# Kernel tuning notes

Measured on AMD Instinct MI355X. Metric: run time of the kernel, lower is better.

Reference implementation:

```python
import jax, jax.numpy as jnp
import numpy as np

B, S, N, D, NAMED, NTYPES = 8, 64, 100, 1024, 768, 5

def _ln(x, g, b, eps=1e-5):
    m = x.mean(-1, keepdims=True)
    v = ((x - m) ** 2).mean(-1, keepdims=True)
    return (x - m) * jax.lax.rsqrt(v + eps) * g + b

def _lin(x, W, b=None):
    y = x @ W.T
    return y if b is None else y + b

def setup_inputs():
    key = jax.random.key(0)
    ks = jax.random.split(key, 24)
    p = lambda i, shape, s=0.02: jax.random.normal(ks[i], shape, jnp.float32) * s
    inp = {}
    inp['scene_reps'] = jax.random.normal(ks[0], (B, S, D), jnp.float32)
    u = jax.random.uniform(ks[1], (B, N, S))
    keep = (jax.random.uniform(ks[2], (B, N, S)) < 0.25).astype(jnp.float32)
    inp['incidence_matrix'] = u * keep
    inp['edge_type_ids'] = jax.random.randint(ks[3], (B, S), 0, NTYPES)
    inp['entity_type_ids'] = jax.random.randint(ks[4], (B, N), 0, NTYPES)
    inp['entity_mask'] = jax.random.uniform(ks[5], (B, N)) < 0.9
    inp['entity_name_embs'] = jax.random.normal(ks[6], (B, N, NAMED), jnp.float32)
    inp['type_embed'] = p(7, (NTYPES, D), 1.0)
    inp['name_W'] = p(8, (D, NAMED))
    inp['name_ln_g'] = jnp.ones(D); inp['name_ln_b'] = jnp.zeros(D)
    inp['n2e_W'] = p(9, (D, D)); inp['n2e_b'] = jnp.zeros(D)
    inp['t2e_W'] = p(10, (D, D)); inp['t2e_b'] = jnp.zeros(D)
    inp['edge_ln_g'] = jnp.ones(D); inp['edge_ln_b'] = jnp.zeros(D)
    inp['gate_W1'] = p(11, (D // 4, D)); inp['gate_b1'] = jnp.zeros(D // 4)
    inp['gate_W2'] = p(12, (3, D // 4)); inp['gate_b2'] = jnp.zeros(3)
    inp['ms_W'] = p(13, (D, D)); inp['ms_b'] = jnp.zeros(D)
    inp['ma_W'] = p(14, (D, D)); inp['ma_b'] = jnp.zeros(D)
    inp['mi_W'] = p(15, (D, D)); inp['mi_b'] = jnp.zeros(D)
    inp['role_w'] = p(16, (D,))
    inp['gru_Wih'] = p(17, (3 * D, D)); inp['gru_Whh'] = p(18, (3 * D, D))
    inp['gru_bih'] = jnp.zeros(3 * D); inp['gru_bhh'] = jnp.zeros(3 * D)
    inp['upd_ln_g'] = jnp.ones(D); inp['upd_ln_b'] = jnp.zeros(D)
    inp['eo_W'] = p(19, (D, D)); inp['eo_b'] = jnp.zeros(D)
    inp['eo_ln_g'] = jnp.ones(D); inp['eo_ln_b'] = jnp.zeros(D)
    inp['res_ln_g'] = jnp.ones(D); inp['res_ln_b'] = jnp.zeros(D)
    return inp

def reference(scene_reps, incidence_matrix, edge_type_ids, entity_type_ids, entity_mask, entity_name_embs, type_embed, name_W, name_ln_g, name_ln_b, n2e_W, n2e_b, t2e_W, t2e_b, edge_ln_g, edge_ln_b, gate_W1, gate_b1, gate_W2, gate_b2, ms_W, ms_b, ma_W, ma_b, mi_W, mi_b, role_w, gru_Wih, gru_Whh, gru_bih, gru_bhh, upd_ln_g, upd_ln_b, eo_W, eo_b, eo_ln_g, eo_ln_b, res_ln_g, res_ln_b):
    # edge_type_ids is accepted by the torch module but unused in its forward.
    dt = scene_reps.dtype
    emaskf = entity_mask.astype(dt)  # [B,N]
    h0 = type_embed[entity_type_ids] + _ln(_lin(entity_name_embs, name_W), name_ln_g, name_ln_b)
    h0 = h0 * emaskf[..., None]
    eye = jnp.eye(N, dtype=dt)
    step_ids = jnp.arange(S)

    def step(carry, xs):
        h, ebuf = carry  # h [B,N,D], ebuf [B,S,D] (hyperedge history)
        s, x_s, inc_s = xs  # x_s [B,D], inc_s [B,N]
        roles = inc_s * emaskf
        wsum = jnp.maximum(roles.sum(1, keepdims=True), 1.0)
        mean_ent = jnp.einsum('bn,bnd->bd', roles, h) / wsum
        e_s = _ln(_lin(mean_ent, n2e_W, n2e_b) + _lin(x_s, t2e_W, t2e_b), edge_ln_g, edge_ln_b)
        in_mask = (roles > 0).astype(dt)[..., None]  # [B,N,1]
        msg_scene = _lin(e_s, ms_W, ms_b)[:, None, :]
        # arc stream: attention over past hyperedges with exponential recency decay
        valid = (step_ids < s).astype(dt)
        denom = jnp.maximum(s - 1, 1).astype(dt)
        decay = jnp.exp(-1.0 + step_ids.astype(dt) / denom) * valid  # linspace(-1,0,s)
        arc = incidence_matrix * roles[:, :, None] * decay[None, None, :]  # [B,N,S]
        arc = arc / jnp.maximum(arc.sum(-1, keepdims=True), 1e-8)
        msg_arc = _lin(jnp.einsum('bns,bsd->bnd', arc, jax.lax.stop_gradient(ebuf)), ma_W, ma_b)
        msg_arc = jnp.where(s > 0, msg_arc, jnp.zeros_like(msg_arc))
        # interaction stream: entity co-occurrence within the scene
        co = roles[:, :, None] * roles[:, None, :] * (1.0 - eye)
        co = co / jnp.maximum(co.sum(-1, keepdims=True), 1e-8)
        msg_int = _lin(jnp.einsum('bnm,bmd->bnd', co, h), mi_W, mi_b)
        gate = jax.nn.softmax(_lin(jax.nn.gelu(_lin(e_s, gate_W1, gate_b1), approximate=False), gate_W2, gate_b2), axis=-1)  # [B,3]
        msg = gate[:, 0, None, None] * msg_scene + gate[:, 1, None, None] * msg_arc + gate[:, 2, None, None] * msg_int
        msg = msg + (roles[..., None] * role_w) * in_mask
        # GRUCell (torch semantics) + LayerNorm, masked update
        gi = _lin(msg, gru_Wih, gru_bih)
        gh = _lin(h, gru_Whh, gru_bhh)
        i_r, i_z, i_n = jnp.split(gi, 3, axis=-1)
        h_r, h_z, h_n = jnp.split(gh, 3, axis=-1)
        r = jax.nn.sigmoid(i_r + h_r)
        z = jax.nn.sigmoid(i_z + h_z)
        n = jnp.tanh(i_n + r * h_n)
        h_new = jnp.clip(_ln((1 - z) * n + z * h, upd_ln_g, upd_ln_b), -50.0, 50.0)
        h = h * (1 - in_mask) + h_new * in_mask
        ebuf = ebuf.at[:, s].set(e_s)
        return (h, ebuf), e_s

    ebuf0 = jnp.zeros((B, S, D), dt)
    (h_fin, _), es = jax.lax.scan(step, (h0, ebuf0), (step_ids, scene_reps.transpose(1, 0, 2), incidence_matrix.transpose(2, 0, 1)))
    H = es.transpose(1, 0, 2)  # [B,S,D]
    H = _ln(H + scene_reps, res_ln_g, res_ln_b)
    H = _ln(jax.nn.gelu(_lin(H, eo_W, eo_b), approximate=False), eo_ln_g, eo_ln_b)
    return (H, h_fin)
```

## Files before the change

### kernel.cpp

```cpp
#include <hip/hip_runtime.h>
#include <math.h>

#define B_   8
#define S_   64
#define N_   100
#define D_   1024
#define ND_  768
#define BN_  800
#define G3_  3072
#define HC7  7168
#define RSC  0.00390625f

typedef _Float16 f16x8 __attribute__((ext_vector_type(8)));
typedef float f32x4 __attribute__((ext_vector_type(4)));

#define MFMA16(a,b,c) __builtin_amdgcn_mfma_f32_16x16x32_f16(a, b, c, 0, 0, 0)

static __device__ __forceinline__ float wave_sum(float v) {
    for (int off = 32; off > 0; off >>= 1) v += __shfl_down(v, off, 64);
    return v;
}

static __device__ __forceinline__ float wave_allsum(float v) {
    for (int off = 1; off < 64; off <<= 1) v += __shfl_xor(v, off, 64);
    return v;
}

static __device__ __forceinline__ float block_sum(float v) {
    __shared__ float red_[8];
    float w = wave_sum(v);
    int lane = threadIdx.x & 63, wid = threadIdx.x >> 6;
    __syncthreads();
    if (lane == 0) red_[wid] = w;
    __syncthreads();
    float t = 0.f;
    for (int i = 0; i < 4; ++i) t += red_[i];
    return t;
}

static __device__ __forceinline__ float gelu_f(float x) {
    return 0.5f * x * (1.f + erff(x * 0.70710678118654752f));
}

static __device__ __forceinline__ unsigned short f2h(float x) {
    union { _Float16 h; unsigned short u; } c; c.h = (_Float16)x; return c.u;
}

__global__ __launch_bounds__(256) void k_f2h(
    const float* __restrict__ src, unsigned short* __restrict__ dst,
    int rows, int cols, int ldd)
{
    size_t n = (size_t)rows * cols;
    size_t i = ((size_t)blockIdx.x * 256 + threadIdx.x) * 4;
    if (i >= n) return;
    int r = (int)(i / cols);
    int c = (int)(i - (size_t)r * cols);
    float4 v = *(const float4*)(src + i);
    ushort4 o; o.x = f2h(v.x); o.y = f2h(v.y); o.z = f2h(v.z); o.w = f2h(v.w);
    *(ushort4*)(dst + (size_t)r * ldd + c) = o;
}

__global__ __launch_bounds__(256) void k_f2hT(
    const float* __restrict__ src, unsigned short* __restrict__ dst,
    int R, int C, int ldd, int rowoff)
{
    __shared__ _Float16 T[32][33];
    int tr = threadIdx.x >> 3, tc4 = (threadIdx.x & 7) * 4;
    int r0 = blockIdx.y * 32, c0 = blockIdx.x * 32;
    float4 v = *(const float4*)(src + (size_t)(r0 + tr) * C + c0 + tc4);
    T[tc4][tr] = (_Float16)v.x; T[tc4+1][tr] = (_Float16)v.y;
    T[tc4+2][tr] = (_Float16)v.z; T[tc4+3][tr] = (_Float16)v.w;
    __syncthreads();
    union { _Float16 h; unsigned short u; } cv;
    ushort4 o;
    cv.h = T[tr][tc4];   o.x = cv.u;
    cv.h = T[tr][tc4+1]; o.y = cv.u;
    cv.h = T[tr][tc4+2]; o.z = cv.u;
    cv.h = T[tr][tc4+3]; o.w = cv.u;
    *(ushort4*)(dst + (size_t)(rowoff + c0 + tr) * ldd + r0 + tc4) = o;
}

__global__ __launch_bounds__(256) void k_mfma16_nt(
    const unsigned short* __restrict__ A16, const unsigned short* __restrict__ W16,
    const float* __restrict__ bias, float* __restrict__ C,
    unsigned short* __restrict__ C16, float oscale,
    int M, int Nc, int K)
{
    int m0 = blockIdx.y * 64; if (m0 >= M) return;
    int n0 = blockIdx.x * 128;
    __shared__ _Float16 sA[64][72];
    __shared__ _Float16 sB[128][72];
    int tid = threadIdx.x;
    int w = tid >> 6, l = tid & 63;
    int l15 = l & 15, q = l >> 4;
    int wn = w * 32;
    int arow = tid >> 3, achk = (tid & 7) * 8;
    f32x4 acc[4][2] = {};
    for (int k0 = 0; k0 < K; k0 += 64) {
        for (int ri = 0; ri < 64; ri += 32) {
            int gm = m0 + arow + ri;
            uint4 v = make_uint4(0u, 0u, 0u, 0u);
            if (gm < M) v = *(const uint4*)(A16 + (size_t)gm * K + k0 + achk);
            *(uint4*)(&sA[arow + ri][achk]) = v;
        }
        for (int i = 0; i < 4; ++i) {
            int r = arow + 32 * i;
            *(uint4*)(&sB[r][achk]) = *(const uint4*)(W16 + (size_t)(n0 + r) * K + k0 + achk);
        }
        __syncthreads();
#pragma unroll
        for (int ks = 0; ks < 64; ks += 32) {
            f16x8 b0 = *(const f16x8*)(&sB[wn + l15][ks + q*8]);
            f16x8 b1 = *(const f16x8*)(&sB[wn + 16 + l15][ks + q*8]);
#pragma unroll
            for (int mi = 0; mi < 4; ++mi) {
                f16x8 a = *(const f16x8*)(&sA[mi*16 + l15][ks + q*8]);
                acc[mi][0] = MFMA16(a, b0, acc[mi][0]);
                acc[mi][1] = MFMA16(a, b1, acc[mi][1]);
            }
        }
        __syncthreads();
    }
    for (int mi = 0; mi < 4; ++mi)
        for (int nj = 0; nj < 2; ++nj)
            for (int r = 0; r < 4; ++r) {
                int gm = m0 + mi*16 + q*4 + r;
                int cl = wn + nj*16 + l15;
                if (gm < M) {
                    size_t off = (size_t)gm * Nc + n0 + cl;
                    float v = acc[mi][nj][r];
                    if (C16) C16[off] = f2h(v * oscale);
                    else C[off] = v + (bias ? bias[n0 + cl] : 0.f);
                }
            }
}

__global__ __launch_bounds__(256) void k_h0(
    const float* __restrict__ P, const int* __restrict__ etype,
    const int* __restrict__ emask, const float* __restrict__ temb,
    const float* __restrict__ g, const float* __restrict__ bt,
    float* __restrict__ h, unsigned short* __restrict__ h16)
{
    int bn = blockIdx.x, tid = threadIdx.x;
    int t = etype[bn], mk = emask[bn];
    float x[4]; float lsum = 0.f;
    for (int k = 0; k < 4; ++k) { x[k] = P[(size_t)bn*D_ + tid + 256*k]; lsum += x[k]; }
    float mean = block_sum(lsum) * (1.f / D_);
    float lv = 0.f;
    for (int k = 0; k < 4; ++k) { float d = x[k] - mean; lv += d * d; }
    float inv = rsqrtf(block_sum(lv) * (1.f / D_) + 1e-5f);
    for (int k = 0; k < 4; ++k) {
        int d = tid + 256*k;
        float y = (x[k] - mean) * inv * g[d] + bt[d];
        float hv = mk ? (temb[(size_t)t*D_ + d] + y) : 0.f;
        h[(size_t)bn*D_ + d] = hv;
        h16[(size_t)bn*D_ + d] = f2h(hv);
    }
}

__global__ __launch_bounds__(256) void k_hcat0(
    const unsigned short* __restrict__ h16, const unsigned short* __restrict__ n2e16,
    const unsigned short* __restrict__ Wmi16, const unsigned short* __restrict__ Whh16,
    float* __restrict__ Hcat)
{
    int m0 = blockIdx.y * 32;
    int n0 = blockIdx.x * 64;
    const unsigned short* Bp; int ldb; int nl;
    if (n0 < 1024)      { Bp = n2e16;        ldb = D_;  nl = n0; }
    else if (n0 < 4096) { Bp = Wmi16 + 2048; ldb = G3_; nl = n0 - 1024; }
    else                { Bp = Whh16;        ldb = D_;  nl = n0 - 4096; }
    __shared__ _Float16 sA[32][72];
    __shared__ _Float16 sB[64][72];
    int tid = threadIdx.x;
    int w = tid >> 6, l = tid & 63;
    int l15 = l & 15, q = l >> 4;
    int wm = (w & 1) * 16, wn = (w >> 1) * 32;
    int arow = tid >> 3, achk = (tid & 7) * 8;
    int gmA = m0 + arow;
    f32x4 acc[2] = {};
    for (int k0 = 0; k0 < D_; k0 += 64) {
        *(uint4*)(&sA[arow][achk]) = *(const uint4*)(h16 + (size_t)gmA*D_ + k0 + achk);
        *(uint4*)(&sB[arow][achk])      = *(const uint4*)(Bp + (size_t)(nl + arow)*ldb + k0 + achk);
        *(uint4*)(&sB[arow + 32][achk]) = *(const uint4*)(Bp + (size_t)(nl + arow + 32)*ldb + k0 + achk);
        __syncthreads();
#pragma unroll
        for (int ks = 0; ks < 64; ks += 32) {
            f16x8 a  = *(const f16x8*)(&sA[wm + l15][ks + q*8]);
            f16x8 b0 = *(const f16x8*)(&sB[wn + l15][ks + q*8]);
            f16x8 b1 = *(const f16x8*)(&sB[wn + 16 + l15][ks + q*8]);
            acc[0] = MFMA16(a, b0, acc[0]);
            acc[1] = MFMA16(a, b1, acc[1]);
        }
        __syncthreads();
    }
    for (int j = 0; j < 2; ++j)
        for (int r = 0; r < 4; ++r) {
            int row = wm + q*4 + r;
            Hcat[(size_t)(m0 + row)*HC7 + n0 + wn + j*16 + l15] = acc[j][r];
        }
}

__global__ __launch_bounds__(256) void k_front(
    const float* __restrict__ inc, const int* __restrict__ emask,
    const float* __restrict__ Esmi, float* __restrict__ arcsum,
    int* __restrict__ cntp, int* __restrict__ lst, float* __restrict__ rro,
    float* __restrict__ scl,
    const int* __restrict__ prevcnt, const int* __restrict__ prevlist,
    const unsigned short* __restrict__ h16, const unsigned short* __restrict__ n2e16,
    const unsigned short* __restrict__ Wmi16, const unsigned short* __restrict__ Whh16,
    float* __restrict__ Hcat, float* __restrict__ gatepre,
    float* __restrict__ esumP, float* __restrict__ TmiP, float* __restrict__ wsumP,
    int s)
{
    int tid = threadIdx.x, bid = blockIdx.x;
    if (bid == 0 && tid < 32) gatepre[tid] = 0.f;
    if (bid < BN_) {
        int m = bid;
        int b = m / N_;
        float r = emask[m] ? inc[(size_t)m*S_ + s] : 0.f;
        if (r <= 0.f) return;
        __shared__ int sidx, nwa;
        __shared__ float wav[S_]; __shared__ int wai[S_];
        if (tid == 0) { sidx = atomicAdd(cntp, 1); nwa = 0; }
        __syncthreads();
        int idx = sidx;
        float denomA = fmaxf((float)(s - 1), 1.f);
        float wa = 0.f;
        if (tid < s) {
            float iv = inc[(size_t)m*S_ + tid];
            if (iv > 0.f) {
                wa = iv * r * expf(-1.f + (float)tid / denomA);
                int p = atomicAdd(&nwa, 1);
                wav[p] = wa; wai[p] = tid;
            }
        }
        float dA = block_sum(wa);
        float rm = 0.f;
        if (tid < N_) rm = emask[b*N_ + tid] ? inc[((size_t)b*N_ + tid)*S_ + s] : 0.f;
        float wsum = block_sum(rm);
        __syncthreads();
        int na = nwa;
        float sclA = 1.f / fmaxf(dA, 1e-8f);
        if (tid == 0) {
            lst[idx] = m; rro[idx] = r;
            scl[idx] = r / fmaxf(r * (wsum - r), 1e-8f);
            wsumP[b] = wsum;
        }
        float rprev = (s > 0) ? inc[(size_t)m*S_ + (s-1)] : 0.f;
        if (rprev <= 0.f) {
            const float4* hp = (const float4*)(Hcat + (size_t)m*HC7);
#pragma unroll
            for (int j2 = 0; j2 < 4; ++j2) {
                float4 hv = hp[tid + 256*j2];
                int c = (tid + 256*j2) * 4;
                float* dst = (c < 1024) ? (esumP + (size_t)b*D_ + c)
                                        : (TmiP + (size_t)b*G3_ + (c - 1024));
                atomicAdd(dst + 0, r*hv.x); atomicAdd(dst + 1, r*hv.y);
                atomicAdd(dst + 2, r*hv.z); atomicAdd(dst + 3, r*hv.w);
            }
        }
        f32x4 a4[3];
#pragma unroll
        for (int k = 0; k < 3; ++k) a4[k] = (f32x4){0.f,0.f,0.f,0.f};
        for (int j = 0; j < na; ++j) {
            float wj = wav[j];
            const f32x4* ep = (const f32x4*)(Esmi + ((size_t)b*S_ + wai[j])*G3_);
#pragma unroll
            for (int k = 0; k < 3; ++k) {
                f32x4 e = ep[tid + 256*k];
#pragma unroll
                for (int q = 0; q < 4; ++q) a4[k][q] += wj * e[q];
            }
        }
        f32x4* ao = (f32x4*)(arcsum + (size_t)idx*G3_);
#pragma unroll
        for (int k = 0; k < 3; ++k) {
            f32x4 v;
#pragma unroll
            for (int q = 0; q < 4; ++q) v[q] = a4[k][q] * sclA;
            ao[tid + 256*k] = v;
        }
    } else {
        int pM = *prevcnt;
        int t = bid - BN_;
        int nt = t % 112, mt = t / 112;
        int m0 = mt * 32;
        if (m0 >= pM) return;
        int n0 = nt * 64;
        const unsigned short* Bp; int ldb; int nl;
        if (n0 < 1024)      { Bp = n2e16;        ldb = D_;  nl = n0; }
        else if (n0 < 4096) { Bp = Wmi16 + 2048; ldb = G3_; nl = n0 - 1024; }
        else                { Bp = Whh16;        ldb = D_;  nl = n0 - 4096; }
        __shared__ _Float16 sA[32][72];
        __shared__ _Float16 sB[64][72];
        __shared__ int slist[32];
        __shared__ float srn[32];
        __shared__ int sbb[32];
        if (tid < 32) {
            int gm = m0 + tid;
            int m = (gm < pM) ? prevlist[gm] : 0;
            slist[tid] = m;
            float rn = 0.f;
            if (gm < pM) rn = emask[m] ? inc[(size_t)m*S_ + s] : 0.f;
            srn[tid] = rn;
            sbb[tid] = m / N_;
        }
        __syncthreads();
        int w = tid >> 6, l = tid & 63;
        int l15 = l & 15, q = l >> 4;
        int wm = (w & 1) * 16, wn = (w >> 1) * 32;
        int arow = tid >> 3, achk = (tid & 7) * 8;
        f32x4 acc[2] = {};
        for (int k0 = 0; k0 < D_; k0 += 64) {
            {
                int gm = m0 + arow;
                uint4 v = make_uint4(0u,0u,0u,0u);
                if (gm < pM) v = *(const uint4*)(h16 + (size_t)slist[arow]*D_ + k0 + achk);
                *(uint4*)(&sA[arow][achk]) = v;
            }
            *(uint4*)(&sB[arow][achk])      = *(const uint4*)(Bp + (size_t)(nl + arow)*ldb + k0 + achk);
            *(uint4*)(&sB[arow + 32][achk]) = *(const uint4*)(Bp + (size_t)(nl + arow + 32)*ldb + k0 + achk);
            __syncthreads();
#pragma unroll
            for (int ks = 0; ks < 64; ks += 32) {
                f16x8 a  = *(const f16x8*)(&sA[wm + l15][ks + q*8]);
                f16x8 b0 = *(const f16x8*)(&sB[wn + l15][ks + q*8]);
                f16x8 b1 = *(const f16x8*)(&sB[wn + 16 + l15][ks + q*8]);
                acc[0] = MFMA16(a, b0, acc[0]);
                acc[1] = MFMA16(a, b1, acc[1]);
            }
            __syncthreads();
        }
        for (int nj = 0; nj < 2; ++nj)
            for (int r4 = 0; r4 < 4; ++r4) {
                int row = wm + q*4 + r4;
                int gm = m0 + row;
                if (gm < pM) {
                    float v = acc[nj][r4];
                    int c = n0 + wn + nj*16 + l15;
                    Hcat[(size_t)slist[row]*HC7 + c] = v;
                    float rn = srn[row];
                    if (rn > 0.f && c < 4096) {
                        float* dst = (c < 1024)
                            ? (esumP + (size_t)sbb[row]*D_ + c)
                            : (TmiP + (size_t)sbb[row]*G3_ + (c - 1024));
                        atomicAdd(dst, rn * v);
                    }
                }
            }
    }
}

__global__ __launch_bounds__(256) void k_mid(
    const float* __restrict__ esumP, const float* __restrict__ wsumP,
    float* __restrict__ esumZ, float* __restrict__ TmiZ, float* __restrict__ wsumZ,
    const float* __restrict__ n2eb, const float* __restrict__ pre_t2e,
    const float* __restrict__ elng, const float* __restrict__ elnb,
    const float* __restrict__ gW1, const float* __restrict__ gb1,
    const float* __restrict__ gW2, const unsigned short* __restrict__ Wmi16,
    float* __restrict__ esbuf, float* __restrict__ gatepre,
    float* __restrict__ Emi, float* __restrict__ Esmi,
    int* __restrict__ ctrl, int par, int s)
{
    int bid = blockIdx.x, tid = threadIdx.x;
    if (bid < 32) {
        __shared__ float se[D_];
        int b = bid >> 2, seg = bid & 3;
        if (bid == 0 && tid == 0) ctrl[1 - par] = 0;
        esumZ[(size_t)b*D_ + seg*256 + tid] = 0.f;
#pragma unroll
        for (int j = 0; j < 3; ++j) TmiZ[(size_t)b*G3_ + seg*768 + j*256 + tid] = 0.f;
        if (seg == 0 && tid == 0) wsumZ[b] = 0.f;
        float invw = 1.f / fmaxf(wsumP[b], 1.f);
        float4 ev = ((const float4*)(esumP + (size_t)b*D_))[tid];
        float4 nb = ((const float4*)n2eb)[tid];
        float4 pt = ((const float4*)(pre_t2e + ((size_t)b*S_ + s)*D_))[tid];
        float x[4] = { ev.x*invw + nb.x + pt.x, ev.y*invw + nb.y + pt.y,
                       ev.z*invw + nb.z + pt.z, ev.w*invw + nb.w + pt.w };
        float mean = block_sum(x[0]+x[1]+x[2]+x[3]) * (1.f / D_);
        float lv = 0.f;
#pragma unroll
        for (int k = 0; k < 4; ++k) { float d = x[k] - mean; lv += d * d; }
        float inv = rsqrtf(block_sum(lv) * (1.f / D_) + 1e-5f);
        float4 lg = ((const float4*)elng)[tid];
        float4 lb = ((const float4*)elnb)[tid];
        float y0 = (x[0]-mean)*inv*lg.x + lb.x;
        float y1 = (x[1]-mean)*inv*lg.y + lb.y;
        float y2 = (x[2]-mean)*inv*lg.z + lb.z;
        float y3 = (x[3]-mean)*inv*lg.w + lb.w;
        int d4 = tid * 4;
        se[d4] = y0; se[d4+1] = y1; se[d4+2] = y2; se[d4+3] = y3;
        if (seg == 0)
            ((float4*)(esbuf + ((size_t)b*S_ + s)*D_))[tid] = make_float4(y0,y1,y2,y3);
        __syncthreads();
        if (tid < 64) {
            int u = seg * 64 + tid;
            float acc = gb1[u];
            const float* w1 = gW1 + (size_t)u * D_;
            for (int j = 0; j < D_; j += 4) {
                float4 w = *(const float4*)(w1 + j);
                acc += w.x*se[j] + w.y*se[j+1] + w.z*se[j+2] + w.w*se[j+3];
            }
            float hg = gelu_f(acc);
            for (int c = 0; c < 3; ++c) {
                float p = wave_sum(gW2[c*256 + u] * hg);
                if (tid == 0) atomicAdd(gatepre + b*4 + c, p);
            }
        }
    } else {
        __shared__ float se32[8][1028];
        int w = tid >> 6, lane = tid & 63;
        for (int bb = 0; bb < 2; ++bb) {
            int b = w*2 + bb;
            float invw = 1.f / fmaxf(wsumP[b], 1.f);
            int d0 = lane * 16;
            const float4* ep = (const float4*)(esumP + (size_t)b*D_ + d0);
            const float4* np = (const float4*)(n2eb + d0);
            const float4* pp = (const float4*)(pre_t2e + ((size_t)b*S_ + s)*D_ + d0);
            float x[16]; float sm = 0.f;
#pragma unroll
            for (int j = 0; j < 4; ++j) {
                float4 e = ep[j], n = np[j], p = pp[j];
                x[j*4+0] = e.x*invw + n.x + p.x;
                x[j*4+1] = e.y*invw + n.y + p.y;
                x[j*4+2] = e.z*invw + n.z + p.z;
// ... 16 lines not shown
                se32[b][d0 + j*4 + 3] = (x[j*4+3]-mean)*inv*lg.w + lb.w;
            }
        }
        __syncthreads();
        int t = bid - 32;
        int seg = t & 1;
        int c0 = (t >> 1) * 32;
        int colg = tid >> 5, t31 = tid & 31;
        int cb = c0 + colg * 4;
        float accA[4][8] = {};
#pragma unroll
        for (int i = 0; i < 8; ++i) {
            int kh = t31*4 + i*128;
            float wf[4][4];
#pragma unroll
            for (int c = 0; c < 4; ++c) {
                union { uint2 u; _Float16 h[4]; } cv;
                cv.u = *(const uint2*)(Wmi16 + (size_t)(cb + c)*G3_ + seg*1024 + kh);
                wf[c][0] = (float)cv.h[0]; wf[c][1] = (float)cv.h[1];
                wf[c][2] = (float)cv.h[2]; wf[c][3] = (float)cv.h[3];
            }
#pragma unroll
            for (int b = 0; b < 8; ++b) {
                float4 sv = *(const float4*)(&se32[b][kh]);
#pragma unroll
                for (int c = 0; c < 4; ++c)
                    accA[c][b] += wf[c][0]*sv.x + wf[c][1]*sv.y
                                + wf[c][2]*sv.z + wf[c][3]*sv.w;
            }
        }
#pragma unroll
        for (int off = 16; off >= 1; off >>= 1) {
#pragma unroll
            for (int c = 0; c < 4; ++c)
#pragma unroll
                for (int b = 0; b < 8; ++b)
                    accA[c][b] += __shfl_down(accA[c][b], off, 32);
        }
        if (t31 == 0) {
#pragma unroll
            for (int c = 0; c < 4; ++c) {
                int col = cb + c;
#pragma unroll
                for (int b = 0; b < 8; ++b) {
                    if (seg == 0) Emi[(size_t)b*G3_ + col] = accA[c][b];
                    else Esmi[((size_t)b*S_ + s)*G3_ + col] = accA[c][b];
                }
            }
        }
    }
}

__global__ __launch_bounds__(256) void k_fin(
    const int* __restrict__ lst, const int* __restrict__ cntp,
    const float* __restrict__ rro, const float* __restrict__ scl,
    const float* __restrict__ gatepre, const float* __restrict__ gb2,
    const float* __restrict__ Hcat, const float* __restrict__ Emi,
    const float* __restrict__ arcsum, const float* __restrict__ Tmi,
    const float* __restrict__ gBm, const float* __restrict__ bih,
    const float* __restrict__ bhh,
    const float* __restrict__ ulng, const float* __restrict__ ulnb,
    float* __restrict__ h, unsigned short* __restrict__ h16, int s)
{
    int row = blockIdx.x;
    if (row >= *cntp) return;
    int bn = lst[row];
    int b = bn / N_;
    int tid = threadIdx.x;
    float t0 = gatepre[b*4+0] + gb2[0];
    float t1 = gatepre[b*4+1] + gb2[1];
    float t2 = gatepre[b*4+2] + gb2[2];
    float mx = fmaxf(t0, fmaxf(t1, t2));
    float e0 = expf(t0-mx), e1 = expf(t1-mx), e2 = expf(t2-mx);
    float si = 1.f / (e0 + e1 + e2);
    float g0 = e0*si, g1 = (s > 0) ? e1*si : 0.f, g2 = e2*si;
    float rv = rro[row];
    float sI = scl[row];
    const f32x4* Hmi4 = (const f32x4*)(Hcat + (size_t)bn*HC7 + 1024);
    const f32x4* Hhh4 = (const f32x4*)(Hcat + (size_t)bn*HC7 + 4096);
    const f32x4* em4  = (const f32x4*)(Emi + (size_t)b*G3_);
    const f32x4* as4  = (const f32x4*)(arcsum + (size_t)row*G3_);
    const f32x4* tm4  = (const f32x4*)(Tmi + (size_t)b*G3_);
    const f32x4* gB4  = (const f32x4*)gBm;
    const f32x4* bih4 = (const f32x4*)bih;
    const f32x4* bhh4 = (const f32x4*)bhh;
    const f32x4* h4   = (const f32x4*)(h + (size_t)bn*D_);
    f32x4 ip[3];
#pragma unroll
    for (int c = 0; c < 3; ++c) {
        int dd4 = c*256 + tid;
        f32x4 tm_ = tm4[dd4], hm_ = Hmi4[dd4], em_ = em4[dd4], as_ = as4[dd4];
        f32x4 b0 = gB4[dd4], b1 = gB4[768 + dd4];
        f32x4 b2 = gB4[1536 + dd4], b3 = gB4[2304 + dd4];
        f32x4 bi = bih4[dd4];
#pragma unroll
        for (int j = 0; j < 4; ++j) {
            float gint = tm_[j] - rv * hm_[j];
            ip[c][j] = RSC * (g0*em_[j] + g1*as_[j] + g2*sI*gint)
                     + g0*b0[j] + g1*b1[j] + g2*b2[j] + rv*b3[j] + bi[j];
        }
    }
    f32x4 a0 = Hhh4[tid],       c0 = bhh4[tid];
    f32x4 a1 = Hhh4[256 + tid], c1 = bhh4[256 + tid];
    f32x4 a2 = Hhh4[512 + tid], c2 = bhh4[512 + tid];
    f32x4 hvv = h4[tid];
    f32x4 u4; float lsum = 0.f;
#pragma unroll
    for (int j = 0; j < 4; ++j) {
        float r = 1.f / (1.f + expf(-(ip[0][j] + a0[j] + c0[j])));
        float z = 1.f / (1.f + expf(-(ip[1][j] + a1[j] + c1[j])));
        float nn = tanhf(ip[2][j] + r * (a2[j] + c2[j]));
        u4[j] = (1.f - z) * nn + z * hvv[j];
        lsum += u4[j];
    }
    float mean = block_sum(lsum) * (1.f / D_);
    float lv = 0.f;
#pragma unroll
    for (int j = 0; j < 4; ++j) { float d = u4[j] - mean; lv += d * d; }
    float inv = rsqrtf(block_sum(lv) * (1.f / D_) + 1e-5f);
    f32x4 lg = ((const f32x4*)ulng)[tid];
    f32x4 lb = ((const f32x4*)ulnb)[tid];
    f32x4 y4; ushort4 o;
#pragma unroll
    for (int j = 0; j < 4; ++j) {
        float y = (u4[j] - mean) * inv * lg[j] + lb[j];
        y4[j] = fminf(fmaxf(y, -50.f), 50.f);
    }
    *(f32x4*)(h + (size_t)bn*D_ + tid*4) = y4;
    o.x = f2h(y4[0]); o.y = f2h(y4[1]); o.z = f2h(y4[2]); o.w = f2h(y4[3]);
    *(ushort4*)(h16 + (size_t)bn*D_ + tid*4) = o;
}

__global__ __launch_bounds__(256) void k_resln(
    float* __restrict__ buf, const float* __restrict__ scene,
    const float* __restrict__ g, const float* __restrict__ bt,
    unsigned short* __restrict__ H16)
{
    size_t row = blockIdx.x;
    int tid = threadIdx.x;
    float x[4]; float lsum = 0.f;
    for (int k = 0; k < 4; ++k) {
        int d = tid + 256*k;
        x[k] = buf[row*D_ + d] + scene[row*D_ + d];
        lsum += x[k];
    }
    float mean = block_sum(lsum) * (1.f / D_);
    float lv = 0.f;
    for (int k = 0; k < 4; ++k) { float d = x[k] - mean; lv += d * d; }
    float inv = rsqrtf(block_sum(lv) * (1.f / D_) + 1e-5f);
    for (int k = 0; k < 4; ++k) {
        int d = tid + 256*k;
        float y = (x[k] - mean) * inv * g[d] + bt[d];
        buf[row*D_ + d] = y;
        H16[row*D_ + d] = f2h(y);
    }
}

__global__ __launch_bounds__(256) void k_final(
    const float* __restrict__ G, const float* __restrict__ g, const float* __restrict__ bt,
    float* __restrict__ outH, const float* __restrict__ h, float* __restrict__ outh)
{
    int tid = threadIdx.x;
    if (blockIdx.x < B_*S_) {
        size_t row = blockIdx.x;
        float x[4]; float lsum = 0.f;
        for (int k = 0; k < 4; ++k) {
            x[k] = gelu_f(G[row*D_ + tid + 256*k]);
            lsum += x[k];
        }
        float mean = block_sum(lsum) * (1.f / D_);
        float lv = 0.f;
        for (int k = 0; k < 4; ++k) { float d = x[k] - mean; lv += d * d; }
        float inv = rsqrtf(block_sum(lv) * (1.f / D_) + 1e-5f);
        for (int k = 0; k < 4; ++k) {
            int d = tid + 256*k;
            outH[row*D_ + d] = (x[k] - mean) * inv * g[d] + bt[d];
        }
    } else {
        size_t bn = blockIdx.x - B_*S_;
        for (int d = tid; d < D_; d += 256)
            outh[bn*D_ + d] = h[bn*D_ + d];
    }
}

extern "C" void kernel_launch(void* const* d_in, const int* in_sizes, int n_in,
                              void* d_out, int out_size, void* d_ws, size_t ws_size,
                              hipStream_t stream)
{
    const float* scene = (const float*)d_in[0];
    const float* inc   = (const float*)d_in[1];
    const int*   etype = (const int*)d_in[3];
    const int*   emask = (const int*)d_in[4];
    const float* nemb  = (const float*)d_in[5];
    const float* temb  = (const float*)d_in[6];
    const float* nameW = (const float*)d_in[7];
    const float* nlg   = (const float*)d_in[8];
    const float* nlb   = (const float*)d_in[9];
    const float* n2eW  = (const float*)d_in[10];
    const float* n2eb  = (const float*)d_in[11];
    const float* t2eW  = (const float*)d_in[12];
    const float* t2eb  = (const float*)d_in[13];
    const float* elng  = (const float*)d_in[14];
    const float* elnb  = (const float*)d_in[15];
    const float* gW1   = (const float*)d_in[16];
    const float* gb1   = (const float*)d_in[17];
    const float* gW2   = (const float*)d_in[18];
    const float* gb2   = (const float*)d_in[19];
    const float* msW   = (const float*)d_in[20];
    const float* msB   = (const float*)d_in[21];
    const float* maW   = (const float*)d_in[22];
    const float* maB   = (const float*)d_in[23];
    const float* miW   = (const float*)d_in[24];
    const float* miB   = (const float*)d_in[25];
    const float* rolew = (const float*)d_in[26];
    const float* Wih   = (const float*)d_in[27];
    const float* Whh   = (const float*)d_in[28];
    const float* bih   = (const float*)d_in[29];
    const float* bhh   = (const float*)d_in[30];
    const float* ulng  = (const float*)d_in[31];
    const float* ulnb  = (const float*)d_in[32];
    const float* eoW   = (const float*)d_in[33];
    const float* eoB   = (const float*)d_in[34];
    const float* eolng = (const float*)d_in[35];
    const float* eolnb = (const float*)d_in[36];
    const float* rlng  = (const float*)d_in[37];
    const float* rlnb  = (const float*)d_in[38];

    float* outH = (float*)d_out;
    float* outh = outH + (size_t)B_*S_*D_;

    float* W = (float*)d_ws;
    size_t o = 0;
    int*   ctrl     = (int*)(W + o); o += 64;
    float* esum2    = W + o; o += 2*(size_t)B_*D_;
    float* Tmi2     = W + o; o += 2*(size_t)B_*G3_;
    float* wsum2    = W + o; o += 16;
    float* gatepre  = W + o; o += 32;
    float* rowrole  = W + o; o += 2*BN_;
    float* sclbuf   = W + o; o += BN_;
    int*   list     = (int*)(W + o); o += 2*BN_;
    float* hbuf     = W + o; o += (size_t)BN_*D_;
    float* Hcat     = W + o; o += (size_t)BN_*HC7;
    float* pre_t2e  = W + o; o += (size_t)B_*S_*D_;
    float* gBm      = W + o; o += 4*G3_;
    float* Emi      = W + o; o += (size_t)B_*G3_;
    float* Esmi     = W + o; o += (size_t)B_*S_*G3_;
    float* arcsum   = W + o; o += (size_t)BN_*G3_;
    float* tmp      = W + o; o += (size_t)BN_*D_;
    unsigned short* U = (unsigned short*)(W + o);
    size_t uo = 0;
    unsigned short* h16    = U + uo; uo += (size_t)BN_*D_;
    unsigned short* H16    = U + uo; uo += (size_t)B_*S_*D_;
    unsigned short* Wih16  = U + uo; uo += (size_t)G3_*D_;
    unsigned short* Whh16  = U + uo; uo += (size_t)G3_*D_;
    unsigned short* n2e16  = U + uo; uo += (size_t)D_*D_;
    unsigned short* eoW16  = U + uo; uo += (size_t)D_*D_;
    unsigned short* nW16   = U + uo; uo += (size_t)D_*ND_;
    unsigned short* nE16   = U + uo; uo += (size_t)BN_*ND_;
    unsigned short* t2e16  = U + uo; uo += (size_t)D_*D_;
    unsigned short* sc16   = U + uo; uo += (size_t)B_*S_*D_;
    unsigned short* WcatT16= U + uo; uo += (size_t)G3_*D_;
    unsigned short* Wmi16  = U + uo; uo += (size_t)G3_*G3_;
    unsigned short* bias4  = U + uo; uo += 4*D_;

    hipMemsetAsync(ctrl, 0,
        (64 + 2*(size_t)B_*D_ + 2*(size_t)B_*G3_ + 16) * sizeof(float), stream);

    #define CVT(src, dst, r, c, ld) \
        k_f2h<<<(((size_t)(r)*(c)/4 + 255)/256), 256, 0, stream>>>(src, dst, r, c, ld)
    CVT(Wih,   Wih16, G3_, D_,  D_);
    CVT(Whh,   Whh16, G3_, D_,  D_);
    CVT(n2eW,  n2e16, D_,  D_,  D_);
    CVT(nameW, nW16,  D_,  ND_, ND_);
    CVT(nemb,  nE16,  BN_, ND_, ND_);
    CVT(eoW,   eoW16, D_,  D_,  D_);
    CVT(t2eW,  t2e16, D_,  D_,  D_);
    CVT(scene, sc16,  B_*S_, D_, D_);
    CVT(msB,   bias4 + 0,    1, D_, D_);
    CVT(maB,   bias4 + D_,   1, D_, D_);
    CVT(miB,   bias4 + 2*D_, 1, D_, D_);
    CVT(rolew, bias4 + 3*D_, 1, D_, D_);
    #undef CVT
    k_f2hT<<<dim3(32,32), 256, 0, stream>>>(msW, WcatT16, D_, D_, D_, 0);
    k_f2hT<<<dim3(32,32), 256, 0, stream>>>(maW, WcatT16, D_, D_, D_, D_);
    k_f2hT<<<dim3(32,32), 256, 0, stream>>>(miW, WcatT16, D_, D_, D_, 2*D_);

    k_mfma16_nt<<<dim3(G3_/128, G3_/64), 256, 0, stream>>>(
        Wih16, WcatT16, nullptr, nullptr, Wmi16, 256.f, G3_, G3_, D_);
    k_mfma16_nt<<<dim3(G3_/128, 1), 256, 0, stream>>>(
        bias4, Wih16, nullptr, gBm, nullptr, 1.f, 4, G3_, D_);
    k_mfma16_nt<<<dim3(D_/128, (B_*S_+63)/64), 256, 0, stream>>>(
        sc16, t2e16, t2eb, pre_t2e, nullptr, 1.f, B_*S_, D_, D_);
    k_mfma16_nt<<<dim3(D_/128, (BN_+63)/64), 256, 0, stream>>>(
        nE16, nW16, nullptr, tmp, nullptr, 1.f, BN_, D_, ND_);
    k_h0<<<BN_, 256, 0, stream>>>(tmp, etype, emask, temb, nlg, nlb, hbuf, h16);
    k_hcat0<<<dim3(112, 25), 256, 0, stream>>>(h16, n2e16, Wmi16, Whh16, Hcat);

    for (int s = 0; s < S_; ++s) {
        int par = s & 1;
        int*   cntp = ctrl + par;
        int*   pcnt = ctrl + (1 - par);
        int*   lst  = list + par * BN_;
        int*   plst = list + (1 - par) * BN_;
        float* rro  = rowrole + par * BN_;
        float* esumP = esum2 + (size_t)par * B_*D_;
        float* esumZ = esum2 + (size_t)(1 - par) * B_*D_;
        float* TmiP  = Tmi2 + (size_t)par * B_*G3_;
        float* TmiZ  = Tmi2 + (size_t)(1 - par) * B_*G3_;
        float* wsumP = wsum2 + par * 8;
        float* wsumZ = wsum2 + (1 - par) * 8;
        k_front<<<BN_ + 112*26, 256, 0, stream>>>(inc, emask, Esmi, arcsum,
            cntp, lst, rro, sclbuf, pcnt, plst, h16, n2e16, Wmi16, Whh16,
            Hcat, gatepre, esumP, TmiP, wsumP, s);
        k_mid<<<224, 256, 0, stream>>>(esumP, wsumP, esumZ, TmiZ, wsumZ,
            n2eb, pre_t2e, elng, elnb, gW1, gb1, gW2, Wmi16,
            outH, gatepre, Emi, Esmi, ctrl, par, s);
        k_fin<<<BN_, 256, 0, stream>>>(lst, cntp, rro, sclbuf, gatepre, gb2,
            Hcat, Emi, arcsum, TmiP, gBm, bih, bhh, ulng, ulnb, hbuf, h16, s);
    }

    k_resln<<<B_*S_, 256, 0, stream>>>(outH, scene, rlng, rlnb, H16);
    k_mfma16_nt<<<dim3(D_/128, (B_*S_+63)/64), 256, 0, stream>>>(
        H16, eoW16, eoB, tmp, nullptr, 1.f, B_*S_, D_, D_);
    k_final<<<B_*S_ + BN_, 256, 0, stream>>>(tmp, eolng, eolnb, outH, hbuf, outh);
}
```

Before: 4.033 ms.

## Accumulate role-weighted hidden sums and project once instead of per-row atomics

Instead of projecting every entity's hidden state through n2e and the Wmi slice and then atomically summing the role-weighted outputs into esum/Tmi, the code now accumulates a role-weighted sum of hidden states per batch (hsum) and multiplies that single vector by the weights in extra blocks of k_front. This removes the n2e columns from the per-row Hcat GEMM and removes the large volume of float atomics on 4096-wide outputs. Accumulation moves into k_fin, which now runs for every entity and adds next-step role-weighted fp16 hidden values. The order of rounding changes slightly, and the small GEMV blocks now run alongside the GEMM tiles.

After: 4.988 ms. 23.7% more time.

```diff
diff --git a/kernel.cpp b/kernel.cpp
--- a/kernel.cpp
+++ b/kernel.cpp
@@ -8,7 +8,8 @@
 #define ND_  768
 #define BN_  800
 #define G3_  3072
-#define HC7  7168
+#define HC6  6144
+#define GMB  2400
 #define RSC  0.00390625f
 
 typedef _Float16 f16x8 __attribute__((ext_vector_type(8)));
@@ -44,6 +45,10 @@
 
 static __device__ __forceinline__ unsigned short f2h(float x) {
     union { _Float16 h; unsigned short u; } c; c.h = (_Float16)x; return c.u;
+}
+
+static __device__ __forceinline__ float h2f(unsigned short u) {
+    union { unsigned short u; _Float16 h; } c; c.u = u; return (float)c.h;
 }
 
 __global__ __launch_bounds__(256) void k_f2h(
@@ -139,10 +144,14 @@
     const float* __restrict__ P, const int* __restrict__ etype,
     const int* __restrict__ emask, const float* __restrict__ temb,
     const float* __restrict__ g, const float* __restrict__ bt,
-    float* __restrict__ h, unsigned short* __restrict__ h16)
+    const float* __restrict__ inc,
+    float* __restrict__ h, unsigned short* __restrict__ h16,
+    float* __restrict__ hsum0)
 {
     int bn = blockIdx.x, tid = threadIdx.x;
     int t = etype[bn], mk = emask[bn];
+    int b = bn / N_;
+    float r0 = mk ? inc[(size_t)bn*S_] : 0.f;
     float x[4]; float lsum = 0.f;
     for (int k = 0; k < 4; ++k) { x[k] = P[(size_t)bn*D_ + tid + 256*k]; lsum += x[k]; }
     float mean = block_sum(lsum) * (1.f / D_);
@@ -154,21 +163,22 @@
         float y = (x[k] - mean) * inv * g[d] + bt[d];
         float hv = mk ? (temb[(size_t)t*D_ + d] + y) : 0.f;
         h[(size_t)bn*D_ + d] = hv;
-        h16[(size_t)bn*D_ + d] = f2h(hv);
+        unsigned short us = f2h(hv);
+        h16[(size_t)bn*D_ + d] = us;
+        if (r0 > 0.f) atomicAdd(hsum0 + (size_t)b*D_ + d, r0 * h2f(us));
     }
 }
 
 __global__ __launch_bounds__(256) void k_hcat0(
-    const unsigned short* __restrict__ h16, const unsigned short* __restrict__ n2e16,
+    const unsigned short* __restrict__ h16,
     const unsigned short* __restrict__ Wmi16, const unsigned short* __restrict__ Whh16,
     float* __restrict__ Hcat)
 {
     int m0 = blockIdx.y * 32;
     int n0 = blockIdx.x * 64;
     const unsigned short* Bp; int ldb; int nl;
-    if (n0 < 1024)      { Bp = n2e16;        ldb = D_;  nl = n0; }
-    else if (n0 < 4096) { Bp = Wmi16 + 2048; ldb = G3_; nl = n0 - 1024; }
-    else                { Bp = Whh16;        ldb = D_;  nl = n0 - 4096; }
+    if (n0 < 3072) { Bp = Wmi16 + 2048; ldb = G3_; nl = n0; }
+    else           { Bp = Whh16;        ldb = D_;  nl = n0 - 3072; }
     __shared__ _Float16 sA[32][72];
     __shared__ _Float16 sB[64][72];
     int tid = threadIdx.x;
@@ -196,20 +206,21 @@
     for (int j = 0; j < 2; ++j)
         for (int r = 0; r < 4; ++r) {
             int row = wm + q*4 + r;
-            Hcat[(size_t)(m0 + row)*HC7 + n0 + wn + j*16 + l15] = acc[j][r];
+            Hcat[(size_t)(m0 + row)*HC6 + n0 + wn + j*16 + l15] = acc[j][r];
         }
 }
 
 __global__ __launch_bounds__(256) void k_front(
     const float* __restrict__ inc, const int* __restrict__ emask,
     const float* __restrict__ Esmi, float* __restrict__ arcsum,
-    int* __restrict__ cntp, int* __restrict__ lst, float* __restrict__ rro,
-    float* __restrict__ scl,
+    int* __restrict__ cntp, int* __restrict__ lst, int* __restrict__ invb,
     const int* __restrict__ prevcnt, const int* __restrict__ prevlist,
     const unsigned short* __restrict__ h16, const unsigned short* __restrict__ n2e16,
     const unsigned short* __restrict__ Wmi16, const unsigned short* __restrict__ Whh16,
     float* __restrict__ Hcat, float* __restrict__ gatepre,
-    float* __restrict__ esumP, float* __restrict__ TmiP, float* __restrict__ wsumP,
+    const float* __restrict__ hsumP,
+    float* __restrict__ esum, float* __restrict__ Tmi,
+    float* __restrict__ wsumP,
     int s)
 {
     int tid = threadIdx.x, bid = blockIdx.x;
@@ -242,22 +253,8 @@
         int na = nwa;
         float sclA = 1.f / fmaxf(dA, 1e-8f);
         if (tid == 0) {
-            lst[idx] = m; rro[idx] = r;
-            scl[idx] = r / fmaxf(r * (wsum - r), 1e-8f);
+            lst[idx] = m; invb[m] = idx;
             wsumP[b] = wsum;
-        }
-        float rprev = (s > 0) ? inc[(size_t)m*S_ + (s-1)] : 0.f;
-        if (rprev <= 0.f) {
-            const float4* hp = (const float4*)(Hcat + (size_t)m*HC7);
-#pragma unroll
-            for (int j2 = 0; j2 < 4; ++j2) {
-                float4 hv = hp[tid + 256*j2];
-                int c = (tid + 256*j2) * 4;
-                float* dst = (c < 1024) ? (esumP + (size_t)b*D_ + c)
-                                        : (TmiP + (size_t)b*G3_ + (c - 1024));
-                atomicAdd(dst + 0, r*hv.x); atomicAdd(dst + 1, r*hv.y);
-                atomicAdd(dst + 2, r*hv.z); atomicAdd(dst + 3, r*hv.w);
-            }
         }
         f32x4 a4[3];
 #pragma unroll
@@ -280,30 +277,22 @@
             for (int q = 0; q < 4; ++q) v[q] = a4[k][q] * sclA;
             ao[tid + 256*k] = v;
         }
-    } else {
+    } else if (bid < BN_ + GMB) {
         int pM = *prevcnt;
         int t = bid - BN_;
-        int nt = t % 112, mt = t / 112;
+        int nt = t % 96, mt = t / 96;
         int m0 = mt * 32;
         if (m0 >= pM) return;
         int n0 = nt * 64;
         const unsigned short* Bp; int ldb; int nl;
-        if (n0 < 1024)      { Bp = n2e16;        ldb = D_;  nl = n0; }
-        else if (n0 < 4096) { Bp = Wmi16 + 2048; ldb = G3_; nl = n0 - 1024; }
-        else                { Bp = Whh16;        ldb = D_;  nl = n0 - 4096; }
+        if (n0 < 3072) { Bp = Wmi16 + 2048; ldb = G3_; nl = n0; }
+        else           { Bp = Whh16;        ldb = D_;  nl = n0 - 3072; }
         __shared__ _Float16 sA[32][72];
         __shared__ _Float16 sB[64][72];
         __shared__ int slist[32];
-        __shared__ float srn[32];
-        __shared__ int sbb[32];
         if (tid < 32) {
             int gm = m0 + tid;
-            int m = (gm < pM) ? prevlist[gm] : 0;
-            slist[tid] = m;
-            float rn = 0.f;
-            if (gm < pM) rn = emask[m] ? inc[(size_t)m*S_ + s] : 0.f;
-            srn[tid] = rn;
-            sbb[tid] = m / N_;
+            slist[tid] = (gm < pM) ? prevlist[gm] : 0;
         }
         __syncthreads();
         int w = tid >> 6, l = tid & 63;
@@ -335,25 +324,62 @@
             for (int r4 = 0; r4 < 4; ++r4) {
                 int row = wm + q*4 + r4;
                 int gm = m0 + row;
-                if (gm < pM) {
-                    float v = acc[nj][r4];
-                    int c = n0 + wn + nj*16 + l15;
-                    Hcat[(size_t)slist[row]*HC7 + c] = v;
-                    float rn = srn[row];
-                    if (rn > 0.f && c < 4096) {
-                        float* dst = (c < 1024)
-                            ? (esumP + (size_t)sbb[row]*D_ + c)
-                            : (TmiP + (size_t)sbb[row]*G3_ + (c - 1024));
-                        atomicAdd(dst, rn * v);
-                    }
+                if (gm < pM)
+                    Hcat[(size_t)slist[row]*HC6 + n0 + wn + nj*16 + l15] = acc[nj][r4];
+            }
+    } else {
+        int t2 = bid - (BN_ + GMB);
+        bool epre = (t2 < 32);
+        int c0 = (epre ? t2 : t2 - 32) * 32;
+        int colg = tid >> 5, t31 = tid & 31;
+        int cb = c0 + colg * 4;
+        float acc[4][8] = {};
+#pragma unroll
+        for (int i = 0; i < 8; ++i) {
+            int kh = t31*4 + i*128;
+            float wf[4][4];
+#pragma unroll
+            for (int c = 0; c < 4; ++c) {
+                union { uint2 u; _Float16 hh[4]; } cv;
+                cv.u = epre
+                    ? *(const uint2*)(n2e16 + (size_t)(cb + c)*D_ + kh)
+                    : *(const uint2*)(Wmi16 + (size_t)(cb + c)*G3_ + 2048 + kh);
+                wf[c][0] = (float)cv.hh[0]; wf[c][1] = (float)cv.hh[1];
+                wf[c][2] = (float)cv.hh[2]; wf[c][3] = (float)cv.hh[3];
+            }
+#pragma unroll
+            for (int b = 0; b < 8; ++b) {
+                float4 hv = *(const float4*)(hsumP + (size_t)b*D_ + kh);
+#pragma unroll
+                for (int c = 0; c < 4; ++c)
+                    acc[c][b] += wf[c][0]*hv.x + wf[c][1]*hv.y
+                               + wf[c][2]*hv.z + wf[c][3]*hv.w;
+            }
+        }
+#pragma unroll
+        for (int off = 16; off >= 1; off >>= 1)
+#pragma unroll
+            for (int c = 0; c < 4; ++c)
+#pragma unroll
+                for (int b = 0; b < 8; ++b)
+                    acc[c][b] += __shfl_down(acc[c][b], off, 32);
+        if (t31 == 0) {
+#pragma unroll
+            for (int c = 0; c < 4; ++c) {
+                int col = cb + c;
+#pragma unroll
+                for (int b = 0; b < 8; ++b) {
+                    if (epre) esum[(size_t)b*D_ + col] = acc[c][b];
+                    else Tmi[(size_t)b*G3_ + col] = acc[c][b];
                 }
             }
+        }
     }
 }
 
 __global__ __launch_bounds__(256) void k_mid(
     const float* __restrict__ esumP, const float* __restrict__ wsumP,
-    float* __restrict__ esumZ, float* __restrict__ TmiZ, float* __restrict__ wsumZ,
+    float* __restrict__ hsumZ,
     const float* __restrict__ n2eb, const float* __restrict__ pre_t2e,
     const float* __restrict__ elng, const float* __restrict__ elnb,
     const float* __restrict__ gW1, const float* __restrict__ gb1,
@@ -367,10 +393,7 @@
         __shared__ float se[D_];
         int b = bid >> 2, seg = bid & 3;
         if (bid == 0 && tid == 0) ctrl[1 - par] = 0;
-        esumZ[(size_t)b*D_ + seg*256 + tid] = 0.f;
-#pragma unroll
-        for (int j = 0; j < 3; ++j) TmiZ[(size_t)b*G3_ + seg*768 + j*256 + tid] = 0.f;
-        if (seg == 0 && tid == 0) wsumZ[b] = 0.f;
+        hsumZ[(size_t)b*D_ + seg*256 + tid] = 0.f;
         float invw = 1.f / fmaxf(wsumP[b], 1.f);
         float4 ev = ((const float4*)(esumP + (size_t)b*D_))[tid];
         float4 nb = ((const float4*)n2eb)[tid];
@@ -493,83 +516,103 @@
 }
 
 __global__ __launch_bounds__(256) void k_fin(
-    const int* __restrict__ lst, const int* __restrict__ cntp,
-    const float* __restrict__ rro, const float* __restrict__ scl,
+    const float* __restrict__ inc, const int* __restrict__ emask,
+    const int* __restrict__ invb,
     const float* __restrict__ gatepre, const float* __restrict__ gb2,
     const float* __restrict__ Hcat, const float* __restrict__ Emi,
     const float* __restrict__ arcsum, const float* __restrict__ Tmi,
+    const float* __restrict__ wsumP,
     const float* __restrict__ gBm, const float* __restrict__ bih,
     const float* __restrict__ bhh,
     const float* __restrict__ ulng, const float* __restrict__ ulnb,
-    float* __restrict__ h, unsigned short* __restrict__ h16, int s)
-{
-    int row = blockIdx.x;
-    if (row >= *cntp) return;
-    int bn = lst[row];
-    int b = bn / N_;
+    float* __restrict__ h, unsigned short* __restrict__ h16,
+    float* __restrict__ hsumN, int s)
+{
+    int m = blockIdx.x;
+    int b = m / N_;
     int tid = threadIdx.x;
-    float t0 = gatepre[b*4+0] + gb2[0];
-    float t1 = gatepre[b*4+1] + gb2[1];
-    float t2 = gatepre[b*4+2] + gb2[2];
-    float mx = fmaxf(t0, fmaxf(t1, t2));
-    float e0 = expf(t0-mx), e1 = expf(t1-mx), e2 = expf(t2-mx);
-    float si = 1.f / (e0 + e1 + e2);
-    float g0 = e0*si, g1 = (s > 0) ? e1*si : 0.f, g2 = e2*si;
-    float rv = rro[row];
-    float sI = scl[row];
-    const f32x4* Hmi4 = (const f32x4*)(Hcat + (size_t)bn*HC7 + 1024);
-    const f32x4* Hhh4 = (const f32x4*)(Hcat + (size_t)bn*HC7 + 4096);
-    const f32x4* em4  = (const f32x4*)(Emi + (size_t)b*G3_);
-    const f32x4* as4  = (const f32x4*)(arcsum + (size_t)row*G3_);
-    const f32x4* tm4  = (const f32x4*)(Tmi + (size_t)b*G3_);
-    const f32x4* gB4  = (const f32x4*)gBm;
-    const f32x4* bih4 = (const f32x4*)bih;
-    const f32x4* bhh4 = (const f32x4*)bhh;
-    const f32x4* h4   = (const f32x4*)(h + (size_t)bn*D_);
-    f32x4 ip[3];
-#pragma unroll
-    for (int c = 0; c < 3; ++c) {
-        int dd4 = c*256 + tid;
-        f32x4 tm_ = tm4[dd4], hm_ = Hmi4[dd4], em_ = em4[dd4], as_ = as4[dd4];
-        f32x4 b0 = gB4[dd4], b1 = gB4[768 + dd4];
-        f32x4 b2 = gB4[1536 + dd4], b3 = gB4[2304 + dd4];
-        f32x4 bi = bih4[dd4];
+    float rv = emask[m] ? inc[(size_t)m*S_ + s] : 0.f;
+    float rn = 0.f;
+    if (s + 1 < S_) rn = emask[m] ? inc[(size_t)m*S_ + s + 1] : 0.f;
+    if (rv > 0.f) {
+        int row = invb[m];
+        float wsum = wsumP[b];
+        float sI = rv / fmaxf(rv * (wsum - rv), 1e-8f);
+        float t0 = gatepre[b*4+0] + gb2[0];
+        float t1 = gatepre[b*4+1] + gb2[1];
+        float t2 = gatepre[b*4+2] + gb2[2];
+        float mx = fmaxf(t0, fmaxf(t1, t2));
+        float e0 = expf(t0-mx), e1 = expf(t1-mx), e2 = expf(t2-mx);
+        float si = 1.f / (e0 + e1 + e2);
+        float g0 = e0*si, g1 = (s > 0) ? e1*si : 0.f, g2 = e2*si;
+        const f32x4* Hmi4 = (const f32x4*)(Hcat + (size_t)m*HC6);
+        const f32x4* Hhh4 = (const f32x4*)(Hcat + (size_t)m*HC6 + 3072);
+        const f32x4* em4  = (const f32x4*)(Emi + (size_t)b*G3_);
+        const f32x4* as4  = (const f32x4*)(arcsum + (size_t)row*G3_);
+        const f32x4* tm4  = (const f32x4*)(Tmi + (size_t)b*G3_);
+        const f32x4* gB4  = (const f32x4*)gBm;
+        const f32x4* bih4 = (const f32x4*)bih;
+        const f32x4* bhh4 = (const f32x4*)bhh;
+        const f32x4* h4   = (const f32x4*)(h + (size_t)m*D_);
+        f32x4 ip[3];
+#pragma unroll
+        for (int c = 0; c < 3; ++c) {
+            int dd4 = c*256 + tid;
+            f32x4 tm_ = tm4[dd4], hm_ = Hmi4[dd4], em_ = em4[dd4], as_ = as4[dd4];
+            f32x4 b0 = gB4[dd4], b1 = gB4[768 + dd4];
+            f32x4 b2 = gB4[1536 + dd4], b3 = gB4[2304 + dd4];
+            f32x4 bi = bih4[dd4];
+#pragma unroll
+            for (int j = 0; j < 4; ++j) {
+                float gint = tm_[j] - rv * hm_[j];
+                ip[c][j] = RSC * (g0*em_[j] + g1*as_[j] + g2*sI*gint)
+                         + g0*b0[j] + g1*b1[j] + g2*b2[j] + rv*b3[j] + bi[j];
+            }
+        }
+        f32x4 a0 = Hhh4[tid],       c0 = bhh4[tid];
+        f32x4 a1 = Hhh4[256 + tid], c1 = bhh4[256 + tid];
+        f32x4 a2 = Hhh4[512 + tid], c2 = bhh4[512 + tid];
+        f32x4 hvv = h4[tid];
+        f32x4 u4; float lsum = 0.f;
 #pragma unroll
         for (int j = 0; j < 4; ++j) {
-            float gint = tm_[j] - rv * hm_[j];
-            ip[c][j] = RSC * (g0*em_[j] + g1*as_[j] + g2*sI*gint)
-                     + g0*b0[j] + g1*b1[j] + g2*b2[j] + rv*b3[j] + bi[j];
-        }
-    }
-    f32x4 a0 = Hhh4[tid],       c0 = bhh4[tid];
-    f32x4 a1 = Hhh4[256 + tid], c1 = bhh4[256 + tid];
-    f32x4 a2 = Hhh4[512 + tid], c2 = bhh4[512 + tid];
-    f32x4 hvv = h4[tid];
-    f32x4 u4; float lsum = 0.f;
-#pragma unroll
-    for (int j = 0; j < 4; ++j) {
-        float r = 1.f / (1.f + expf(-(ip[0][j] + a0[j] + c0[j])));
-        float z = 1.f / (1.f + expf(-(ip[1][j] + a1[j] + c1[j])));
-        float nn = tanhf(ip[2][j] + r * (a2[j] + c2[j]));
-        u4[j] = (1.f - z) * nn + z * hvv[j];
-        lsum += u4[j];
-    }
-    float mean = block_sum(lsum) * (1.f / D_);
-    float lv = 0.f;
-#pragma unroll
-    for (int j = 0; j < 4; ++j) { float d = u4[j] - mean; lv += d * d; }
-    float inv = rsqrtf(block_sum(lv) * (1.f / D_) + 1e-5f);
-    f32x4 lg = ((const f32x4*)ulng)[tid];
-    f32x4 lb = ((const f32x4*)ulnb)[tid];
-    f32x4 y4; ushort4 o;
-#pragma unroll
-    for (int j = 0; j < 4; ++j) {
-        float y = (u4[j] - mean) * inv * lg[j] + lb[j];
-        y4[j] = fminf(fmaxf(y, -50.f), 50.f);
-    }
-    *(f32x4*)(h + (size_t)bn*D_ + tid*4) = y4;
-    o.x = f2h(y4[0]); o.y = f2h(y4[1]); o.z = f2h(y4[2]); o.w = f2h(y4[3]);
-    *(ushort4*)(h16 + (size_t)bn*D_ + tid*4) = o;
+            float r = 1.f / (1.f + expf(-(ip[0][j] + a0[j] + c0[j])));
+            float z = 1.f / (1.f + expf(-(ip[1][j] + a1[j] + c1[j])));
+            float nn = tanhf(ip[2][j] + r * (a2[j] + c2[j]));
+            u4[j] = (1.f - z) * nn + z * hvv[j];
+            lsum += u4[j];
+        }
+        float mean = block_sum(lsum) * (1.f / D_);
+        float lv = 0.f;
+#pragma unroll
+        for (int j = 0; j < 4; ++j) { float d = u4[j] - mean; lv += d * d; }
+        float inv = rsqrtf(block_sum(lv) * (1.f / D_) + 1e-5f);
+        f32x4 lg = ((const f32x4*)ulng)[tid];
+        f32x4 lb = ((const f32x4*)ulnb)[tid];
+        f32x4 y4; ushort4 o;
+#pragma unroll
+        for (int j = 0; j < 4; ++j) {
+            float y = (u4[j] - mean) * inv * lg[j] + lb[j];
+            y4[j] = fminf(fmaxf(y, -50.f), 50.f);
+        }
+        *(f32x4*)(h + (size_t)m*D_ + tid*4) = y4;
+        o.x = f2h(y4[0]); o.y = f2h(y4[1]); o.z = f2h(y4[2]); o.w = f2h(y4[3]);
+        *(ushort4*)(h16 + (size_t)m*D_ + tid*4) = o;
+        if (rn > 0.f) {
+            float* dst = hsumN + (size_t)b*D_ + tid*4;
+            atomicAdd(dst + 0, rn * h2f(o.x));
+            atomicAdd(dst + 1, rn * h2f(o.y));
+            atomicAdd(dst + 2, rn * h2f(o.z));
+            atomicAdd(dst + 3, rn * h2f(o.w));
+        }
+    } else if (rn > 0.f) {
+        ushort4 o = *(const ushort4*)(h16 + (size_t)m*D_ + tid*4);
+        float* dst = hsumN + (size_t)b*D_ + tid*4;
+        atomicAdd(dst + 0, rn * h2f(o.x));
+        atomicAdd(dst + 1, rn * h2f(o.y));
+        atomicAdd(dst + 2, rn * h2f(o.z));
+        atomicAdd(dst + 3, rn * h2f(o.w));
+    }
 }
 
 __global__ __launch_bounds__(256) void k_resln(
@@ -673,20 +716,20 @@
     float* W = (float*)d_ws;
     size_t o = 0;
     int*   ctrl     = (int*)(W + o); o += 64;
-    float* esum2    = W + o; o += 2*(size_t)B_*D_;
-    float* Tmi2     = W + o; o += 2*(size_t)B_*G3_;
-    float* wsum2    = W + o; o += 16;
+    float* hsum2    = W + o; o += 2*(size_t)B_*D_;
+    float* wsumB    = W + o; o += 16;
     float* gatepre  = W + o; o += 32;
-    float* rowrole  = W + o; o += 2*BN_;
-    float* sclbuf   = W + o; o += BN_;
     int*   list     = (int*)(W + o); o += 2*BN_;
+    int*   invb     = (int*)(W + o); o += BN_;
     float* hbuf     = W + o; o += (size_t)BN_*D_;
-    float* Hcat     = W + o; o += (size_t)BN_*HC7;
+    float* Hcat     = W + o; o += (size_t)BN_*HC6;
     float* pre_t2e  = W + o; o += (size_t)B_*S_*D_;
     float* gBm      = W + o; o += 4*G3_;
     float* Emi      = W + o; o += (size_t)B_*G3_;
     float* Esmi     = W + o; o += (size_t)B_*S_*G3_;
     float* arcsum   = W + o; o += (size_t)BN_*G3_;
+    float* esum     = W + o; o += (size_t)B_*D_;
+    float* Tmi      = W + o; o += (size_t)B_*G3_;
     float* tmp      = W + o; o += (size_t)BN_*D_;
     unsigned short* U = (unsigned short*)(W + o);
     size_t uo = 0;
@@ -704,8 +747,7 @@
     unsigned short* Wmi16  = U + uo; uo += (size_t)G3_*G3_;
     unsigned short* bias4  = U + uo; uo += 4*D_;
 
-    hipMemsetAsync(ctrl, 0,
-        (64 + 2*(size_t)B_*D_ + 2*(size_t)B_*G3_ + 16) * sizeof(float), stream);
+    hipMemsetAsync(ctrl, 0, (64 + 2*(size_t)B_*D_ + 16) * sizeof(float), stream);
 
     #define CVT(src, dst, r, c, ld) \
         k_f2h<<<(((size_t)(r)*(c)/4 + 255)/256), 256, 0, stream>>>(src, dst, r, c, ld)
@@ -734,30 +776,27 @@
         sc16, t2e16, t2eb, pre_t2e, nullptr, 1.f, B_*S_, D_, D_);
     k_mfma16_nt<<<dim3(D_/128, (BN_+63)/64), 256, 0, stream>>>(
         nE16, nW16, nullptr, tmp, nullptr, 1.f, BN_, D_, ND_);
-    k_h0<<<BN_, 256, 0, stream>>>(tmp, etype, emask, temb, nlg, nlb, hbuf, h16);
-    k_hcat0<<<dim3(112, 25), 256, 0, stream>>>(h16, n2e16, Wmi16, Whh16, Hcat);
+    k_h0<<<BN_, 256, 0, stream>>>(tmp, etype, emask, temb, nlg, nlb, inc,
+                                  hbuf, h16, hsum2);
+    k_hcat0<<<dim3(96, 25), 256, 0, stream>>>(h16, Wmi16, Whh16, Hcat);
 
     for (int s = 0; s < S_; ++s) {
-        int par = s & 1;
+        int par = s & 1, parn = 1 - par;
         int*   cntp = ctrl + par;
-        int*   pcnt = ctrl + (1 - par);
+        int*   pcnt = ctrl + parn;
         int*   lst  = list + par * BN_;
-        int*   plst = list + (1 - par) * BN_;
-        float* rro  = rowrole + par * BN_;
-        float* esumP = esum2 + (size_t)par * B_*D_;
-        float* esumZ = esum2 + (size_t)(1 - par) * B_*D_;
-        float* TmiP  = Tmi2 + (size_t)par * B_*G3_;
-        float* TmiZ  = Tmi2 + (size_t)(1 - par) * B_*G3_;
-        float* wsumP = wsum2 + par * 8;
-        float* wsumZ = wsum2 + (1 - par) * 8;
-        k_front<<<BN_ + 112*26, 256, 0, stream>>>(inc, emask, Esmi, arcsum,
-            cntp, lst, rro, sclbuf, pcnt, plst, h16, n2e16, Wmi16, Whh16,
-            Hcat, gatepre, esumP, TmiP, wsumP, s);
-        k_mid<<<224, 256, 0, stream>>>(esumP, wsumP, esumZ, TmiZ, wsumZ,
+        int*   plst = list + parn * BN_;
+        float* hsumP = hsum2 + (size_t)par * B_*D_;
+        float* hsumN = hsum2 + (size_t)parn * B_*D_;
+        k_front<<<BN_ + GMB + 128, 256, 0, stream>>>(inc, emask, Esmi, arcsum,
+            cntp, lst, invb, pcnt, plst, h16, n2e16, Wmi16, Whh16,
+            Hcat, gatepre, hsumP, esum, Tmi, wsumB, s);
+        k_mid<<<224, 256, 0, stream>>>(esum, wsumB, hsumN,
             n2eb, pre_t2e, elng, elnb, gW1, gb1, gW2, Wmi16,
             outH, gatepre, Emi, Esmi, ctrl, par, s);
-        k_fin<<<BN_, 256, 0, stream>>>(lst, cntp, rro, sclbuf, gatepre, gb2,
-            Hcat, Emi, arcsum, TmiP, gBm, bih, bhh, ulng, ulnb, hbuf, h16, s);
+        k_fin<<<BN_, 256, 0, stream>>>(inc, emask, invb, gatepre, gb2,
+            Hcat, Emi, arcsum, Tmi, wsumB, gBm, bih, bhh, ulng, ulnb,
+            hbuf, h16, hsumN, s);
     }
 
     k_resln<<<B_*S_, 256, 0, stream>>>(outH, scene, rlng, rlnb, H16);
```
